# Kernel tuning notes

Measured on AMD Instinct MI355X. Metric: run time of the kernel, lower is better.

The kernel has to match this reference:

```python
import jax, jax.numpy as jnp
import numpy as np

N = 50000          # nodes
E = 800000         # edges (before self-loops)
IN = 128           # in_channels
C = 32             # hidden_channels
H = 4              # heads
SLOPE = 0.2        # PyG GATConv default negative_slope
NUM_CLASSES = 2


def setup_inputs() -> dict:
    key = jax.random.key(0)
    ks = jax.random.split(key, 20)
    s = 0.1
    inp = {
        "x": jax.random.normal(ks[0], (N, IN), jnp.float32),
        "edge_index": jax.random.randint(ks[1], (2, E), 0, N, jnp.int64),
        # conv1: IN -> H*C (concat)
        "W1": jax.random.normal(ks[2], (IN, H * C), jnp.float32) * s,
        "a1_src": jax.random.normal(ks[3], (H, C), jnp.float32) * s,
        "a1_dst": jax.random.normal(ks[4], (H, C), jnp.float32) * s,
        "b1": jnp.zeros((H * C,), jnp.float32),
        # conv2: H*C -> H*C (concat)
        "W2": jax.random.normal(ks[5], (H * C, H * C), jnp.float32) * s,
        "a2_src": jax.random.normal(ks[6], (H, C), jnp.float32) * s,
        "a2_dst": jax.random.normal(ks[7], (H, C), jnp.float32) * s,
        "b2": jnp.zeros((H * C,), jnp.float32),
        # conv3: H*C -> C (heads=1, concat=False)
        "W3": jax.random.normal(ks[8], (H * C, C), jnp.float32) * s,
        "a3_src": jax.random.normal(ks[9], (1, C), jnp.float32) * s,
        "a3_dst": jax.random.normal(ks[10], (1, C), jnp.float32) * s,
        "b3": jnp.zeros((C,), jnp.float32),
        # node classification head: C -> 2
        "Wc": jax.random.normal(ks[11], (C, NUM_CLASSES), jnp.float32) * s,
        "bc": jnp.zeros((NUM_CLASSES,), jnp.float32),
    }
    return inp


def gat_conv(x, src, dst, W, a_src, a_dst, b, heads, out_c, concat):
    """PyG-style GATConv with self-loops already appended to (src, dst)."""
    n = x.shape[0]
    h = (x @ W).reshape(n, heads, out_c)            # [N,H,C]
    al_src = jnp.sum(h * a_src, axis=-1)            # [N,H]
    al_dst = jnp.sum(h * a_dst, axis=-1)            # [N,H]
    e = al_src[src] + al_dst[dst]                   # [Et,H]
    e = jax.nn.leaky_relu(e, SLOPE)
    # numerically-stable segment softmax over edges sharing a destination
    emax = jax.ops.segment_max(e, dst, num_segments=n)   # every node has a self-loop
    e = jnp.exp(e - emax[dst])
    denom = jax.ops.segment_sum(e, dst, num_segments=n)
    alpha = e / (denom[dst] + 1e-16)                # [Et,H]
    msg = h[src] * alpha[:, :, None]                # [Et,H,C]
    out = jax.ops.segment_sum(msg, dst, num_segments=n)  # [N,H,C]
    out = out.reshape(n, heads * out_c) if concat else jnp.mean(out, axis=1)
    return out + b


def reference(x, edge_index, W1, a1_src, a1_dst, b1, W2, a2_src, a2_dst, b2,
              W3, a3_src, a3_dst, b3, Wc, bc):
    n = x.shape[0]
    loop = jnp.arange(n, dtype=edge_index.dtype)
    src = jnp.concatenate([edge_index[0], loop])
    dst = jnp.concatenate([edge_index[1], loop])
    h = jax.nn.elu(gat_conv(x, src, dst, W1, a1_src, a1_dst, b1, H, C, True))
    h = jax.nn.elu(gat_conv(h, src, dst, W2, a2_src, a2_dst, b2, H, C, True))
    h = gat_conv(h, src, dst, W3, a3_src, a3_dst, b3, 1, C, False)
    node_output = h @ Wc + bc                       # [N,2]
    link_embedding = h                              # [N,C]
    return (node_output, link_embedding)
```

## Files before the change

### kernel.cpp

```cpp
#include <hip/hip_runtime.h>
#include <math.h>

#define SLOPE 0.2f

__device__ __forceinline__ float lrelu(float x) { return x > 0.f ? x : SLOPE * x; }

__device__ __forceinline__ float bflo(unsigned int u) { return __uint_as_float(u << 16); }
__device__ __forceinline__ float bfhi(unsigned int u) { return __uint_as_float(u & 0xffff0000u); }
__device__ __forceinline__ unsigned short f2bf(float f) {
    unsigned int u = __float_as_uint(f);
    unsigned int r = u + 0x7fffu + ((u >> 16) & 1u);
    return (unsigned short)(r >> 16);
}

typedef short frag8 __attribute__((ext_vector_type(8)));
typedef float f32x4 __attribute__((ext_vector_type(4)));

__global__ __launch_bounds__(256) void wtrans_kernel(
    const float* __restrict__ W1, const float* __restrict__ W2,
    unsigned short* __restrict__ Wt1, unsigned short* __restrict__ Wt2)
{
    int idx = blockIdx.x * 256 + threadIdx.x;
    const float* W = W1;
    unsigned short* Wt = Wt1;
    int i = idx;
    if (idx >= 16384) { W = W2; Wt = Wt2; i = idx - 16384; }
    int n = i >> 7, k = i & 127;
    Wt[i] = f2bf(W[k * 128 + n]);
}

template <bool BF16IN>
__global__ __launch_bounds__(256) void transform_mfma_kernel(
    const void* __restrict__ xin, const unsigned short* __restrict__ Wt,
    const float* __restrict__ a_src, const float* __restrict__ a_dst,
    unsigned short* __restrict__ hout, float* __restrict__ alsrc,
    float* __restrict__ aldst, int N)
{
    constexpr int MB = 64;
    constexpr int LDK = 136;
    __shared__ __align__(16) unsigned short xs[MB * LDK];
    __shared__ __align__(16) unsigned short wt[128 * LDK];

    const int node0 = blockIdx.x * MB;
    const int t = threadIdx.x;

    if constexpr (BF16IN) {
        const unsigned short* xb = (const unsigned short*)xin;
        for (int i = t; i < MB * 16; i += 256) {
            int row = i >> 4, c16 = i & 15;
            uint4 v = make_uint4(0u, 0u, 0u, 0u);
            if (node0 + row < N)
                v = ((const uint4*)(xb + (size_t)(node0 + row) * 128))[c16];
            *(uint4*)&xs[row * LDK + c16 * 8] = v;
        }
    } else {
        const float* xf = (const float*)xin;
        for (int i = t; i < MB * 32; i += 256) {
            int row = i >> 5, col4 = i & 31;
            ushort4 o;
            if (node0 + row < N) {
                float4 v = ((const float4*)(xf + (size_t)(node0 + row) * 128))[col4];
                o.x = f2bf(v.x); o.y = f2bf(v.y); o.z = f2bf(v.z); o.w = f2bf(v.w);
            } else {
                o.x = o.y = o.z = o.w = 0;
            }
            *(ushort4*)&xs[row * LDK + col4 * 4] = o;
        }
    }
    for (int i = t; i < 2048; i += 256) {
        int n = i >> 4, k16 = i & 15;
        uint4 v = ((const uint4*)Wt)[i];
        *(uint4*)&wt[n * LDK + k16 * 8] = v;
    }
    __syncthreads();

    const int w    = t >> 6;
    const int lane = t & 63;
    const int r    = lane & 15;
    const int q    = lane >> 4;

    f32x4 acc[4][2];
#pragma unroll
    for (int mt = 0; mt < 4; ++mt)
#pragma unroll
        for (int nl = 0; nl < 2; ++nl)
            acc[mt][nl] = (f32x4){0.f, 0.f, 0.f, 0.f};

#pragma unroll
    for (int kk = 0; kk < 4; ++kk) {
        const int kof = kk * 32 + q * 8;
        frag8 b0 = *(const frag8*)&wt[(w * 32 + r) * LDK + kof];
        frag8 b1 = *(const frag8*)&wt[(w * 32 + 16 + r) * LDK + kof];
#pragma unroll
        for (int mt = 0; mt < 4; ++mt) {
            frag8 a = *(const frag8*)&xs[(mt * 16 + r) * LDK + kof];
            acc[mt][0] = __builtin_amdgcn_mfma_f32_16x16x32_bf16(a, b0, acc[mt][0], 0, 0, 0);
            acc[mt][1] = __builtin_amdgcn_mfma_f32_16x16x32_bf16(a, b1, acc[mt][1], 0, 0, 0);
        }
    }

    const float as0 = a_src[w * 32 + r],      ad0 = a_dst[w * 32 + r];
    const float as1 = a_src[w * 32 + 16 + r], ad1 = a_dst[w * 32 + 16 + r];
#pragma unroll
    for (int mt = 0; mt < 4; ++mt) {
#pragma unroll
        for (int reg = 0; reg < 4; ++reg) {
            float s = acc[mt][0][reg] * as0 + acc[mt][1][reg] * as1;
            float d = acc[mt][0][reg] * ad0 + acc[mt][1][reg] * ad1;
#pragma unroll
            for (int off = 1; off < 16; off <<= 1) {
                s += __shfl_xor(s, off);
                d += __shfl_xor(d, off);
            }
            if (r == 0) {
                int m = mt * 16 + q * 4 + reg;
                int n = node0 + m;
                if (n < N) {
                    alsrc[n * 4 + w] = s;
                    aldst[n * 4 + w] = d;
                }
            }
        }
    }

    __syncthreads();
#pragma unroll
    for (int mt = 0; mt < 4; ++mt)
#pragma unroll
        for (int nl = 0; nl < 2; ++nl)
#pragma unroll
            for (int reg = 0; reg < 4; ++reg) {
                int m = mt * 16 + q * 4 + reg;
                int n = w * 32 + nl * 16 + r;
                xs[m * LDK + n] = f2bf(acc[mt][nl][reg]);
            }
    __syncthreads();
    {
        int row = t >> 2, cbase = (t & 3) * 32;
        if (node0 + row < N) {
            uint4* dst = (uint4*)(hout + (size_t)(node0 + row) * 128 + cbase);
#pragma unroll
            for (int j = 0; j < 4; ++j)
                dst[j] = *(const uint4*)&xs[row * LDK + cbase + j * 8];
        }
    }
}

template <int COUT, int Hh, int NPT>
__global__ __launch_bounds__(256) void transform_kernel(
    const unsigned short* __restrict__ xin, const float* __restrict__ W,
    const float* __restrict__ a_src, const float* __restrict__ a_dst,
    unsigned short* __restrict__ hout, float* __restrict__ alsrc,
    float* __restrict__ aldst, int N)
{
    constexpr int JT = COUT / 4;
    constexpr int GROUPS = 256 / JT;
    constexpr int NB = GROUPS * NPT;
    constexpr int PAD = 4;
    __shared__ __align__(16) float xs[NB][128 + PAD];

    const int node0 = blockIdx.x * NB;
    for (int i = threadIdx.x; i < NB * 16; i += 256) {
        int row = i >> 4, c16 = i & 15;
        uint4 v = make_uint4(0u, 0u, 0u, 0u);
        if (node0 + row < N)
            v = ((const uint4*)(xin + (size_t)(node0 + row) * 128))[c16];
        float* xp = &xs[row][c16 * 8];
        xp[0] = bflo(v.x); xp[1] = bfhi(v.x);
        xp[2] = bflo(v.y); xp[3] = bfhi(v.y);
        xp[4] = bflo(v.z); xp[5] = bfhi(v.z);
        xp[6] = bflo(v.w); xp[7] = bfhi(v.w);
    }
    __syncthreads();

    const int jt = threadIdx.x % JT;
    const int g  = threadIdx.x / JT;
    const int j4 = jt * 4;

    float4 acc[NPT];
#pragma unroll
    for (int m = 0; m < NPT; ++m) acc[m] = make_float4(0.f, 0.f, 0.f, 0.f);

    const float4* Wf4 = (const float4*)W;
    for (int k4 = 0; k4 < 32; ++k4) {
        float4 w0 = Wf4[(4 * k4 + 0) * JT + jt];
        float4 w1 = Wf4[(4 * k4 + 1) * JT + jt];
        float4 w2 = Wf4[(4 * k4 + 2) * JT + jt];
        float4 w3 = Wf4[(4 * k4 + 3) * JT + jt];
#pragma unroll
        for (int m = 0; m < NPT; ++m) {
            float4 xv = *(const float4*)&xs[g * NPT + m][k4 << 2];
            acc[m].x += xv.x * w0.x + xv.y * w1.x + xv.z * w2.x + xv.w * w3.x;
            acc[m].y += xv.x * w0.y + xv.y * w1.y + xv.z * w2.y + xv.w * w3.y;
            acc[m].z += xv.x * w0.z + xv.y * w1.z + xv.z * w2.z + xv.w * w3.z;
            acc[m].w += xv.x * w0.w + xv.y * w1.w + xv.z * w2.w + xv.w * w3.w;
        }
    }

    const float4 as4 = ((const float4*)a_src)[jt];
    const float4 ad4 = ((const float4*)a_dst)[jt];
    const int hh = j4 >> 5;

#pragma unroll
    for (int m = 0; m < NPT; ++m) {
        int n = node0 + g * NPT + m;
        float4 v = acc[m];
        float sv = v.x * as4.x + v.y * as4.y + v.z * as4.z + v.w * as4.w;
        float dv = v.x * ad4.x + v.y * ad4.y + v.z * ad4.z + v.w * ad4.w;
#pragma unroll
        for (int off = 4; off >= 1; off >>= 1) {
            sv += __shfl_xor(sv, off);
            dv += __shfl_xor(dv, off);
        }
        if (n < N) {
            ushort4 hp;
            hp.x = f2bf(v.x); hp.y = f2bf(v.y);
            hp.z = f2bf(v.z); hp.w = f2bf(v.w);
            ((ushort4*)(hout + (size_t)n * COUT))[jt] = hp;
            if ((jt & 7) == 0) {
                alsrc[n * Hh + hh] = sv;
                aldst[n * Hh + hh] = dv;
            }
        }
    }
}

#define BKT_CAP 2048
#define NBKT_MAX 1024
#define CH_BIN 4096

__global__ __launch_bounds__(1024) void bin_kernel(
    const int* __restrict__ src, const int* __restrict__ dst,
    int* __restrict__ bcnt, unsigned int* __restrict__ tmp, int E, int nbkt)
{
    __shared__ int hist[NBKT_MAX];
    __shared__ int base[NBKT_MAX];
    const int e0 = blockIdx.x * CH_BIN;
    const int e1 = min(e0 + CH_BIN, E);

    for (int b = threadIdx.x; b < nbkt; b += 1024) hist[b] = 0;
    __syncthreads();
    for (int e = e0 + threadIdx.x; e < e1; e += 1024) {
        int d = __builtin_nontemporal_load(dst + e);
        atomicAdd(&hist[d >> 6], 1);
    }
    __syncthreads();
    for (int b = threadIdx.x; b < nbkt; b += 1024) {
        int c = hist[b];
        base[b] = (c > 0) ? atomicAdd(&bcnt[b << 4], c) : 0;
        hist[b] = 0;
    }
    __syncthreads();
    for (int e = e0 + threadIdx.x; e < e1; e += 1024) {
        int d = __builtin_nontemporal_load(dst + e);
        int s = __builtin_nontemporal_load(src + e);
        int b = d >> 6;
        int pos = base[b] + atomicAdd(&hist[b], 1);
        if (pos < BKT_CAP)
            tmp[((size_t)b << 11) + pos] =
                ((unsigned int)s << 6) | (unsigned int)(d & 63);
    }
}

__global__ __launch_bounds__(256) void bucket_csr_kernel(
    const unsigned int* __restrict__ tmp, const int* __restrict__ bcnt,
    int* __restrict__ deg, int* __restrict__ offsets,
    int* __restrict__ src_sorted, int N)
{
    int b = blockIdx.x;
    __shared__ int hist[64];
    if (threadIdx.x < 64) hist[threadIdx.x] = 0;
    __syncthreads();
    int cnt = min(bcnt[b << 4], BKT_CAP);
    const unsigned int* tb = tmp + ((size_t)b << 11);
    for (int i = threadIdx.x; i < cnt; i += 256)
        atomicAdd(&hist[tb[i] & 63u], 1);
    __syncthreads();
    if (threadIdx.x < 64) {
        int v = hist[threadIdx.x];
        int incl = v;
#pragma unroll
        for (int off = 1; off < 64; off <<= 1) {
            int t2 = __shfl_up(incl, off);
            if (threadIdx.x >= off) incl += t2;
        }
        int excl = incl - v;
        int node = (b << 6) + threadIdx.x;
        if (node < N) {
            deg[node] = v;
            offsets[node] = (b << 11) + excl;
        }
        hist[threadIdx.x] = excl;
    }
    __syncthreads();
    for (int i = threadIdx.x; i < cnt; i += 256) {
        unsigned int p = tb[i];
        int pos = atomicAdd(&hist[p & 63u], 1);
        src_sorted[((size_t)b << 11) + pos] = (int)(p >> 6);
    }
}

__device__ __forceinline__ void fma8(const uint4& p, float w, float* a) {
    a[0] += w * bflo(p.x); a[1] += w * bfhi(p.x);
    a[2] += w * bflo(p.y); a[3] += w * bfhi(p.y);
    a[4] += w * bflo(p.z); a[5] += w * bfhi(p.z);
    a[6] += w * bflo(p.w); a[7] += w * bfhi(p.w);
}

template <int Hh, int Cc, bool DO_ELU, bool OUTBF, bool FUSE_HEAD>
__global__ __launch_bounds__(256) void gat_agg_kernel(
    const int* __restrict__ offsets, const int* __restrict__ deg_arr,
    const int* __restrict__ src_sorted,
    const unsigned short* __restrict__ h, const float* __restrict__ alsrc,
    const float* __restrict__ aldst, const float* __restrict__ bias,
    void* __restrict__ outv, const float* __restrict__ Wc,
    const float* __restrict__ bc, float* __restrict__ node_out, int N)
{
    constexpr int HC  = Hh * Cc;
    constexpr int TPN = HC / 8;
    constexpr int NPB = 256 / TPN;
    constexpr int CHUNK = 64;
    __shared__ int   s_src[NPB][CHUNK];
    __shared__ __align__(16) float s_w[NPB][CHUNK][Hh];
    __shared__ int   s_nch[NPB];

    const int g  = threadIdx.x / TPN;
    const int lt = threadIdx.x % TPN;
    const int n  = blockIdx.x * NPB + g;
    const bool valid = n < N;

    int off0 = 0, deg = 0;
    if (valid) { off0 = offsets[n]; deg = deg_arr[n]; }
    if (lt == 0) s_nch[g] = (deg + CHUNK - 1) / CHUNK;
    __syncthreads();
    int maxch = 0;
#pragma unroll
    for (int i = 0; i < NPB; ++i) maxch = max(maxch, s_nch[i]);

    const int hh = (lt * 8) / Cc;
    float adv[Hh];
    if (valid) {
        if constexpr (Hh == 4) {
            float4 t = ((const float4*)aldst)[n];
            adv[0] = t.x; adv[1] = t.y; adv[2] = t.z; adv[3] = t.w;
        } else {
            adv[0] = aldst[n];
        }
    }

    const uint4* h4 = (const uint4*)h;

    float a[8] = {0.f, 0.f, 0.f, 0.f, 0.f, 0.f, 0.f, 0.f};
    float den = 0.f;
    for (int ch = 0; ch < maxch; ++ch) {
        int base = ch * CHUNK;
        int cnt = deg - base;
        cnt = cnt < 0 ? 0 : (cnt > CHUNK ? CHUNK : cnt);
        __syncthreads();
        for (int i = lt; i < cnt; i += TPN) {
            int s = src_sorted[off0 + base + i];
            s_src[g][i] = s;
            if constexpr (Hh == 4) {
                float4 av = ((const float4*)alsrc)[s];
                ((float4*)&s_w[g][i][0])[0] = make_float4(
                    __expf(lrelu(av.x + adv[0])), __expf(lrelu(av.y + adv[1])),
                    __expf(lrelu(av.z + adv[2])), __expf(lrelu(av.w + adv[3])));
            } else {
                s_w[g][i][0] = __expf(lrelu(alsrc[s] + adv[0]));
            }
        }
        __syncthreads();
        int i = 0;
        for (; i + 1 < cnt; i += 2) {
            int s0 = s_src[g][i], s1 = s_src[g][i + 1];
            float w0 = s_w[g][i][hh], w1 = s_w[g][i + 1][hh];
            uint4 p0 = h4[(size_t)s0 * TPN + lt];
            uint4 p1 = h4[(size_t)s1 * TPN + lt];
            fma8(p0, w0, a);
            fma8(p1, w1, a);
            den += w0 + w1;
        }
        if (i < cnt) {
            int s0 = s_src[g][i];
            float w0 = s_w[g][i][hh];
            uint4 p0 = h4[(size_t)s0 * TPN + lt];
            fma8(p0, w0, a);
            den += w0;
        }
    }

    if (valid) {
        float wself = __expf(lrelu(alsrc[n * Hh + hh] + adv[hh]));
        uint4 p = h4[(size_t)n * TPN + lt];
        fma8(p, wself, a);
        den += wself + 1e-16f;
        float inv = 1.f / den;
        float4 bv0 = ((const float4*)bias)[lt * 2];
        float4 bv1 = ((const float4*)bias)[lt * 2 + 1];
        float o[8];
        o[0] = a[0] * inv + bv0.x; o[1] = a[1] * inv + bv0.y;
        o[2] = a[2] * inv + bv0.z; o[3] = a[3] * inv + bv0.w;
        o[4] = a[4] * inv + bv1.x; o[5] = a[5] * inv + bv1.y;
        o[6] = a[6] * inv + bv1.z; o[7] = a[7] * inv + bv1.w;
        if (DO_ELU) {
#pragma unroll
            for (int q = 0; q < 8; ++q)
                o[q] = o[q] > 0.f ? o[q] : __expf(o[q]) - 1.f;
        }
        if constexpr (OUTBF) {
            unsigned short* ob = (unsigned short*)outv;
            uint4 pk;
            pk.x = (unsigned int)f2bf(o[0]) | ((unsigned int)f2bf(o[1]) << 16);
            pk.y = (unsigned int)f2bf(o[2]) | ((unsigned int)f2bf(o[3]) << 16);
            pk.z = (unsigned int)f2bf(o[4]) | ((unsigned int)f2bf(o[5]) << 16);
            pk.w = (unsigned int)f2bf(o[6]) | ((unsigned int)f2bf(o[7]) << 16);
            ((uint4*)(ob + (size_t)n * HC))[lt] = pk;
        } else {
            float* of = (float*)outv;
            float4* op = (float4*)(of + (size_t)n * HC);
            op[lt * 2]     = make_float4(o[0], o[1], o[2], o[3]);
            op[lt * 2 + 1] = make_float4(o[4], o[5], o[6], o[7]);
        }
        if constexpr (FUSE_HEAD) {
            float s0 = 0.f, s1 = 0.f;
#pragma unroll
            for (int q = 0; q < 8; ++q) {
                int c = lt * 8 + q;
                s0 += o[q] * Wc[c * 2];
                s1 += o[q] * Wc[c * 2 + 1];
            }
            s0 += __shfl_xor(s0, 1); s0 += __shfl_xor(s0, 2);
            s1 += __shfl_xor(s1, 1); s1 += __shfl_xor(s1, 2);
            if (lt == 0) {
                node_out[(size_t)n * 2]     = s0 + bc[0];
                node_out[(size_t)n * 2 + 1] = s1 + bc[1];
            }
        }
    }
}

extern "C" void kernel_launch(void* const* d_in, const int* in_sizes, int n_in,
                              void* d_out, int out_size, void* d_ws, size_t ws_size,
                              hipStream_t stream)
{
    const float* x   = (const float*)d_in[0];
    const int*   ei  = (const int*)d_in[1];
    const float* W1  = (const float*)d_in[2];
    const float* a1s = (const float*)d_in[3];
    const float* a1d = (const float*)d_in[4];
    const float* b1  = (const float*)d_in[5];
    const float* W2  = (const float*)d_in[6];
    const float* a2s = (const float*)d_in[7];
    const float* a2d = (const float*)d_in[8];
    const float* b2  = (const float*)d_in[9];
    const float* W3  = (const float*)d_in[10];
    const float* a3s = (const float*)d_in[11];
    const float* a3d = (const float*)d_in[12];
    const float* b3  = (const float*)d_in[13];
    const float* Wc  = (const float*)d_in[14];
    const float* bc  = (const float*)d_in[15];

    const int N = in_sizes[0] / 128;
    const int E = in_sizes[1] / 2;
    const int* srcIdx = ei;
    const int* dstIdx = ei + E;

    const int NBKT = (N + 63) >> 6;

    float* alsrc = (float*)d_ws;
    float* aldst = alsrc + (size_t)N * 4;
    unsigned short* fb16 = (unsigned short*)(aldst + (size_t)N * 4);
    unsigned short* hbuf = fb16 + (size_t)N * 128;
    int* deg        = (int*)(hbuf + (size_t)N * 128);
    int* offsets    = deg + N;
    uintptr_t wp = ((uintptr_t)(offsets + N) + 15) & ~(uintptr_t)15;
    unsigned short* wt1 = (unsigned short*)wp;
    unsigned short* wt2 = wt1 + 16384;
    int* bcnt       = (int*)(wt2 + 16384);
    int* src_sorted = bcnt + (size_t)NBKT * 16;
    unsigned int* tmp = (unsigned int*)(src_sorted + (size_t)NBKT * BKT_CAP);

    float* node_out = (float*)d_out;
    float* link_out = node_out + (size_t)N * 2;

    const int nbBin = (E + CH_BIN - 1) / CH_BIN;

    wtrans_kernel<<<128, 256, 0, stream>>>(W1, W2, wt1, wt2);
    hipMemsetAsync(bcnt, 0, (size_t)NBKT * 16 * sizeof(int), stream);
    bin_kernel<<<nbBin, 1024, 0, stream>>>(srcIdx, dstIdx, bcnt, tmp, E, NBKT);
    bucket_csr_kernel<<<NBKT, 256, 0, stream>>>(tmp, bcnt, deg, offsets, src_sorted, N);

    transform_mfma_kernel<false><<<(N + 63) / 64, 256, 0, stream>>>(
        x, wt1, a1s, a1d, hbuf, alsrc, aldst, N);
    gat_agg_kernel<4, 32, true, true, false><<<(N + 15) / 16, 256, 0, stream>>>(
        offsets, deg, src_sorted, hbuf, alsrc, aldst, b1, fb16,
        nullptr, nullptr, nullptr, N);

    transform_mfma_kernel<true><<<(N + 63) / 64, 256, 0, stream>>>(
        fb16, wt2, a2s, a2d, hbuf, alsrc, aldst, N);
    gat_agg_kernel<4, 32, true, true, false><<<(N + 15) / 16, 256, 0, stream>>>(
        offsets, deg, src_sorted, hbuf, alsrc, aldst, b2, fb16,
        nullptr, nullptr, nullptr, N);

    transform_kernel<32, 1, 4><<<(N + 127) / 128, 256, 0, stream>>>(
        fb16, W3, a3s, a3d, hbuf, alsrc, aldst, N);
    gat_agg_kernel<1, 32, false, false, true><<<(N + 63) / 64, 256, 0, stream>>>(
        offsets, deg, src_sorted, hbuf, alsrc, aldst, b3, link_out,
        Wc, bc, node_out, N);
}
```

Before: 271.5 us.

## Merge CSR build with layer-1 transform, fold memset, restructure aggregation weights

Zeroing of the bucket counters moves into the weight-transpose kernel, which removes a separate memset launch. The bucket-to-CSR pass and the first MFMA feature transform become one kernel that dispatches by block index, so these two independent jobs run concurrently and one launch is saved. In the aggregation kernel, attention weights are stored head-planar with padding so four weights load as one float4. The edge loop is unrolled by 4, and the self-loop row is prefetched early. The fused kernel gives the CSR blocks the transform's large shared-memory footprint, which may lower their occupancy.

```diff
diff --git a/kernel.cpp b/kernel.cpp
--- a/kernel.cpp
+++ b/kernel.cpp
@@ -18,9 +18,11 @@
 
 __global__ __launch_bounds__(256) void wtrans_kernel(
     const float* __restrict__ W1, const float* __restrict__ W2,
-    unsigned short* __restrict__ Wt1, unsigned short* __restrict__ Wt2)
+    unsigned short* __restrict__ Wt1, unsigned short* __restrict__ Wt2,
+    int* __restrict__ bcnt, int nbcnt)
 {
     int idx = blockIdx.x * 256 + threadIdx.x;
+    if (idx < nbcnt) bcnt[idx] = 0;
     const float* W = W1;
     unsigned short* Wt = Wt1;
     int i = idx;
@@ -29,19 +31,21 @@
     Wt[i] = f2bf(W[k * 128 + n]);
 }
 
+#define TF_MB 64
+#define TF_LDK 136
+
 template <bool BF16IN>
-__global__ __launch_bounds__(256) void transform_mfma_kernel(
-    const void* __restrict__ xin, const unsigned short* __restrict__ Wt,
+__device__ __forceinline__ void transform_body(
+    int bid, const void* __restrict__ xin, const unsigned short* __restrict__ Wt,
     const float* __restrict__ a_src, const float* __restrict__ a_dst,
     unsigned short* __restrict__ hout, float* __restrict__ alsrc,
-    float* __restrict__ aldst, int N)
-{
-    constexpr int MB = 64;
-    constexpr int LDK = 136;
-    __shared__ __align__(16) unsigned short xs[MB * LDK];
-    __shared__ __align__(16) unsigned short wt[128 * LDK];
-
-    const int node0 = blockIdx.x * MB;
+    float* __restrict__ aldst, int N,
+    unsigned short* xs, unsigned short* wt)
+{
+    constexpr int MB = TF_MB;
+    constexpr int LDK = TF_LDK;
+
+    const int node0 = bid * MB;
     const int t = threadIdx.x;
 
     if constexpr (BF16IN) {
@@ -144,6 +148,19 @@
                 dst[j] = *(const uint4*)&xs[row * LDK + cbase + j * 8];
         }
     }
+}
+
+template <bool BF16IN>
+__global__ __launch_bounds__(256) void transform_mfma_kernel(
+    const void* __restrict__ xin, const unsigned short* __restrict__ Wt,
+    const float* __restrict__ a_src, const float* __restrict__ a_dst,
+    unsigned short* __restrict__ hout, float* __restrict__ alsrc,
+    float* __restrict__ aldst, int N)
+{
+    __shared__ __align__(16) unsigned short xs[TF_MB * TF_LDK];
+    __shared__ __align__(16) unsigned short wt[128 * TF_LDK];
+    transform_body<BF16IN>(blockIdx.x, xin, Wt, a_src, a_dst, hout,
+                           alsrc, aldst, N, xs, wt);
 }
 
 template <int COUT, int Hh, int NPT>
@@ -262,13 +279,11 @@
     }
 }
 
-__global__ __launch_bounds__(256) void bucket_csr_kernel(
-    const unsigned int* __restrict__ tmp, const int* __restrict__ bcnt,
+__device__ __forceinline__ void bucket_csr_body(
+    int b, const unsigned int* __restrict__ tmp, const int* __restrict__ bcnt,
     int* __restrict__ deg, int* __restrict__ offsets,
-    int* __restrict__ src_sorted, int N)
-{
-    int b = blockIdx.x;
-    __shared__ int hist[64];
+    int* __restrict__ src_sorted, int N, int* hist)
+{
     if (threadIdx.x < 64) hist[threadIdx.x] = 0;
     __syncthreads();
     int cnt = min(bcnt[b << 4], BKT_CAP);
@@ -282,7 +297,7 @@
 #pragma unroll
         for (int off = 1; off < 64; off <<= 1) {
             int t2 = __shfl_up(incl, off);
-            if (threadIdx.x >= off) incl += t2;
+            if ((int)threadIdx.x >= off) incl += t2;
         }
         int excl = incl - v;
         int node = (b << 6) + threadIdx.x;
@@ -297,6 +312,25 @@
         unsigned int p = tb[i];
         int pos = atomicAdd(&hist[p & 63u], 1);
         src_sorted[((size_t)b << 11) + pos] = (int)(p >> 6);
+    }
+}
+
+template <bool BF16IN>
+__global__ __launch_bounds__(256) void csr_transform_kernel(
+    const unsigned int* __restrict__ tmp, const int* __restrict__ bcnt,
+    int* __restrict__ deg, int* __restrict__ offsets, int* __restrict__ src_sorted,
+    const void* __restrict__ xin, const unsigned short* __restrict__ Wt,
+    const float* __restrict__ a_src, const float* __restrict__ a_dst,
+    unsigned short* __restrict__ hout, float* __restrict__ alsrc,
+    float* __restrict__ aldst, int N, int nbkt)
+{
+    __shared__ __align__(16) unsigned short smem[TF_MB * TF_LDK + 128 * TF_LDK];
+    if ((int)blockIdx.x < nbkt) {
+        bucket_csr_body(blockIdx.x, tmp, bcnt, deg, offsets, src_sorted, N,
+                        (int*)smem);
+    } else {
+        transform_body<BF16IN>(blockIdx.x - nbkt, xin, Wt, a_src, a_dst,
+                               hout, alsrc, aldst, N, smem, smem + TF_MB * TF_LDK);
     }
 }
 
@@ -320,8 +354,10 @@
     constexpr int TPN = HC / 8;
     constexpr int NPB = 256 / TPN;
     constexpr int CHUNK = 64;
+    constexpr int CH_STRIDE = CHUNK + 4;
+    constexpr int PLANE = NPB * CH_STRIDE + 8;
     __shared__ int   s_src[NPB][CHUNK];
-    __shared__ __align__(16) float s_w[NPB][CHUNK][Hh];
+    __shared__ __align__(16) float s_w[Hh * PLANE];
     __shared__ int   s_nch[NPB];
 
     const int g  = threadIdx.x / TPN;
@@ -349,6 +385,15 @@
     }
 
     const uint4* h4 = (const uint4*)h;
+
+    uint4 pself = make_uint4(0u, 0u, 0u, 0u);
+    float als_self = 0.f;
+    if (valid) {
+        pself = h4[(size_t)n * TPN + lt];
+        als_self = alsrc[n * Hh + hh];
+    }
+
+    const int wbase = hh * PLANE + g * CH_STRIDE;
 
     float a[8] = {0.f, 0.f, 0.f, 0.f, 0.f, 0.f, 0.f, 0.f};
     float den = 0.f;
@@ -362,27 +407,33 @@
             s_src[g][i] = s;
             if constexpr (Hh == 4) {
                 float4 av = ((const float4*)alsrc)[s];
-                ((float4*)&s_w[g][i][0])[0] = make_float4(
-                    __expf(lrelu(av.x + adv[0])), __expf(lrelu(av.y + adv[1])),
-                    __expf(lrelu(av.z + adv[2])), __expf(lrelu(av.w + adv[3])));
+                s_w[0 * PLANE + g * CH_STRIDE + i] = __expf(lrelu(av.x + adv[0]));
+                s_w[1 * PLANE + g * CH_STRIDE + i] = __expf(lrelu(av.y + adv[1]));
+                s_w[2 * PLANE + g * CH_STRIDE + i] = __expf(lrelu(av.z + adv[2]));
+                s_w[3 * PLANE + g * CH_STRIDE + i] = __expf(lrelu(av.w + adv[3]));
             } else {
-                s_w[g][i][0] = __expf(lrelu(alsrc[s] + adv[0]));
+                s_w[g * CH_STRIDE + i] = __expf(lrelu(alsrc[s] + adv[0]));
             }
         }
         __syncthreads();
         int i = 0;
-        for (; i + 1 < cnt; i += 2) {
-            int s0 = s_src[g][i], s1 = s_src[g][i + 1];
-            float w0 = s_w[g][i][hh], w1 = s_w[g][i + 1][hh];
+        for (; i + 3 < cnt; i += 4) {
+            int s0 = s_src[g][i],     s1 = s_src[g][i + 1];
+            int s2 = s_src[g][i + 2], s3 = s_src[g][i + 3];
+            float4 wv = *(const float4*)&s_w[wbase + i];
             uint4 p0 = h4[(size_t)s0 * TPN + lt];
             uint4 p1 = h4[(size_t)s1 * TPN + lt];
-            fma8(p0, w0, a);
-            fma8(p1, w1, a);
-            den += w0 + w1;
-        }
-        if (i < cnt) {
+            uint4 p2 = h4[(size_t)s2 * TPN + lt];
+            uint4 p3 = h4[(size_t)s3 * TPN + lt];
+            fma8(p0, wv.x, a);
+            fma8(p1, wv.y, a);
+            fma8(p2, wv.z, a);
+            fma8(p3, wv.w, a);
+            den += (wv.x + wv.y) + (wv.z + wv.w);
+        }
+        for (; i < cnt; ++i) {
             int s0 = s_src[g][i];
-            float w0 = s_w[g][i][hh];
+            float w0 = s_w[wbase + i];
             uint4 p0 = h4[(size_t)s0 * TPN + lt];
             fma8(p0, w0, a);
             den += w0;
@@ -390,9 +441,8 @@
     }
 
     if (valid) {
-        float wself = __expf(lrelu(alsrc[n * Hh + hh] + adv[hh]));
-        uint4 p = h4[(size_t)n * TPN + lt];
-        fma8(p, wself, a);
+        float wself = __expf(lrelu(als_self + adv[hh]));
+        fma8(pself, wself, a);
         den += wself + 1e-16f;
         float inv = 1.f / den;
         float4 bv0 = ((const float4*)bias)[lt * 2];
@@ -484,19 +534,21 @@
     float* link_out = node_out + (size_t)N * 2;
 
     const int nbBin = (E + CH_BIN - 1) / CH_BIN;
-
-    wtrans_kernel<<<128, 256, 0, stream>>>(W1, W2, wt1, wt2);
-    hipMemsetAsync(bcnt, 0, (size_t)NBKT * 16 * sizeof(int), stream);
+    const int nbT   = (N + 63) / 64;
+
+    wtrans_kernel<<<128, 256, 0, stream>>>(W1, W2, wt1, wt2, bcnt, NBKT * 16);
+
     bin_kernel<<<nbBin, 1024, 0, stream>>>(srcIdx, dstIdx, bcnt, tmp, E, NBKT);
-    bucket_csr_kernel<<<NBKT, 256, 0, stream>>>(tmp, bcnt, deg, offsets, src_sorted, N);
-
-    transform_mfma_kernel<false><<<(N + 63) / 64, 256, 0, stream>>>(
-        x, wt1, a1s, a1d, hbuf, alsrc, aldst, N);
+
+    csr_transform_kernel<false><<<NBKT + nbT, 256, 0, stream>>>(
+        tmp, bcnt, deg, offsets, src_sorted,
+        x, wt1, a1s, a1d, hbuf, alsrc, aldst, N, NBKT);
+
     gat_agg_kernel<4, 32, true, true, false><<<(N + 15) / 16, 256, 0, stream>>>(
         offsets, deg, src_sorted, hbuf, alsrc, aldst, b1, fb16,
         nullptr, nullptr, nullptr, N);
 
-    transform_mfma_kernel<true><<<(N + 63) / 64, 256, 0, stream>>>(
+    transform_mfma_kernel<true><<<nbT, 256, 0, stream>>>(
         fb16, wt2, a2s, a2d, hbuf, alsrc, aldst, N);
     gat_agg_kernel<4, 32, true, true, false><<<(N + 15) / 16, 256, 0, stream>>>(
         offsets, deg, src_sorted, hbuf, alsrc, aldst, b2, fb16,
```

New measurement: 272.1 us. No clear change (+0.2%).
